# Kernel optimization log

Measured on AMD Instinct MI355X. Metric: run time of the kernel, lower is better.

Reference implementation:

```python
import jax, jax.numpy as jnp
import numpy as np

B, D, H, W, C = 2, 28, 28, 28, 96
HEADS = 3
WS = (7, 7, 7)
SS = (3, 3, 3)
N = WS[0] * WS[1] * WS[2]  # 343 tokens per window
MLP_DIM = 4 * C


def _rel_pos_index():
    coords = np.stack(np.meshgrid(np.arange(WS[0]), np.arange(WS[1]), np.arange(WS[2]), indexing='ij'))
    cf = coords.reshape(3, -1)
    rel = (cf[:, :, None] - cf[:, None, :]).transpose(1, 2, 0)
    rel[..., 0] += WS[0] - 1
    rel[..., 1] += WS[1] - 1
    rel[..., 2] += WS[2] - 1
    rel[..., 0] *= (2 * WS[1] - 1) * (2 * WS[2] - 1)
    rel[..., 1] *= 2 * WS[2] - 1
    return rel.sum(-1)  # [N, N] int


def _compute_mask():
    # shifted-window attention mask (MONAI compute_mask)
    img = np.zeros((1, D, H, W, 1), np.float32)
    cnt = 0.0
    for ds in (slice(0, -WS[0]), slice(-WS[0], -SS[0]), slice(-SS[0], None)):
        for hs in (slice(0, -WS[1]), slice(-WS[1], -SS[1]), slice(-SS[1], None)):
            for ws_ in (slice(0, -WS[2]), slice(-WS[2], -SS[2]), slice(-SS[2], None)):
                img[:, ds, hs, ws_, :] = cnt
                cnt += 1.0
    mw = img.reshape(1, D // WS[0], WS[0], H // WS[1], WS[1], W // WS[2], WS[2], 1)
    mw = mw.transpose(0, 1, 3, 5, 2, 4, 6, 7).reshape(-1, N)  # [nw, N]
    diff = mw[:, None, :] - mw[:, :, None]
    return np.where(diff != 0, -100.0, 0.0).astype(np.float32)  # [nw, N, N]


def _ln(x, g, b):
    mu = x.mean(-1, keepdims=True)
    var = ((x - mu) ** 2).mean(-1, keepdims=True)
    return (x - mu) * jax.lax.rsqrt(var + 1e-5) * g + b


def setup_inputs() -> dict:
    key = jax.random.key(0)
    ks = jax.random.split(key, 8)
    f = lambda k, shape: (jax.random.normal(k, shape) * 0.02).astype(jnp.float32)
    n_bias = (2 * WS[0] - 1) * (2 * WS[1] - 1) * (2 * WS[2] - 1)
    return {
        'x': jax.random.normal(ks[0], (B, D, H, W, C), jnp.float32),
        'mask_matrix': jnp.asarray(_compute_mask()),
        'g1': jnp.ones((C,), jnp.float32), 'b1': jnp.zeros((C,), jnp.float32),
        'w_qkv': f(ks[1], (3 * C, C)), 'b_qkv': jnp.zeros((3 * C,), jnp.float32),
        'bias_table': f(ks[2], (n_bias, HEADS)),
        'w_proj': f(ks[3], (C, C)), 'b_proj': jnp.zeros((C,), jnp.float32),
        'g2': jnp.ones((C,), jnp.float32), 'b2': jnp.zeros((C,), jnp.float32),
        'w_fc1': f(ks[4], (MLP_DIM, C)), 'b_fc1': jnp.zeros((MLP_DIM,), jnp.float32),
        'w_fc2': f(ks[5], (C, MLP_DIM)), 'b_fc2': jnp.zeros((C,), jnp.float32),
        'rel_index': jnp.asarray(_rel_pos_index(), dtype=jnp.int32),
    }


def reference(x, mask_matrix, g1, b1, w_qkv, b_qkv, bias_table, w_proj, b_proj,
              g2, b2, w_fc1, b_fc1, w_fc2, b_fc2, rel_index):
    shortcut = x
    h = _ln(x, g1, b1)
    # cyclic shift
    h = jnp.roll(h, (-SS[0], -SS[1], -SS[2]), axis=(1, 2, 3))
    # window partition -> [B_, N, C]
    win = h.reshape(B, D // WS[0], WS[0], H // WS[1], WS[1], W // WS[2], WS[2], C)
    win = win.transpose(0, 1, 3, 5, 2, 4, 6, 7).reshape(-1, N, C)
    Bw = win.shape[0]
    hd = C // HEADS
    qkv = (win @ w_qkv.T + b_qkv).reshape(Bw, N, 3, HEADS, hd).transpose(2, 0, 3, 1, 4)
    q, k, v = qkv[0] * (hd ** -0.5), qkv[1], qkv[2]
    attn = jnp.einsum('bhnd,bhmd->bhnm', q, k)  # [Bw, H, N, N]
    bias = bias_table[rel_index.reshape(-1)].reshape(N, N, HEADS).transpose(2, 0, 1)
    attn = attn + bias[None]
    nw = mask_matrix.shape[0]
    attn = attn.reshape(Bw // nw, nw, HEADS, N, N) + mask_matrix[None, :, None]
    attn = jax.nn.softmax(attn.reshape(Bw, HEADS, N, N), axis=-1)
    out = jnp.einsum('bhnm,bhmd->bhnd', attn, v).transpose(0, 2, 1, 3).reshape(Bw, N, C)
    out = out @ w_proj.T + b_proj
    # window reverse -> [B, D, H, W, C]
    out = out.reshape(B, D // WS[0], H // WS[1], W // WS[2], WS[0], WS[1], WS[2], C)
    out = out.transpose(0, 1, 4, 2, 5, 3, 6, 7).reshape(B, D, H, W, C)
    # reverse cyclic shift
    out = jnp.roll(out, SS, axis=(1, 2, 3))
    x = shortcut + out
    h2 = _ln(x, g2, b2)
    h2 = jax.nn.gelu(h2 @ w_fc1.T + b_fc1, approximate=False)
    return x + (h2 @ w_fc2.T + b_fc2)
```

## Files before the change

kernel.cpp:

```cpp
#include <hip/hip_runtime.h>
#include <hip/hip_bf16.h>
#include <math.h>

typedef unsigned short u16;
typedef unsigned int u32;
typedef unsigned char u8;

#define T_TOK 43904
#define NTOK 343
#define LOG2E 1.4426950408889634f
#define MASKV 144.26950408889634f

typedef __attribute__((ext_vector_type(4))) float f32x4;
typedef __attribute__((ext_vector_type(8))) short s16x8;

__device__ __forceinline__ float bf2f(u32 v) { return __uint_as_float(v << 16); }
__device__ __forceinline__ u16 f2bf(float f) {
  u32 u = __float_as_uint(f);
  return (u16)((u + 0x7fffu + ((u >> 16) & 1u)) >> 16);
}

__device__ __forceinline__ float ldf(const void* p, int f32, size_t i) {
  return f32 ? ((const float*)p)[i] : bf2f(((const u16*)p)[i]);
}
__device__ __forceinline__ void ld8(const void* p, int f32, size_t i, float* o) {
  if (f32) {
    float4 a = *(const float4*)((const float*)p + i);
    float4 b = *(const float4*)((const float*)p + i + 4);
    o[0] = a.x; o[1] = a.y; o[2] = a.z; o[3] = a.w;
    o[4] = b.x; o[5] = b.y; o[6] = b.z; o[7] = b.w;
  } else {
    uint4 pk = *(const uint4*)((const u16*)p + i);
    u32 v[4] = {pk.x, pk.y, pk.z, pk.w};
    #pragma unroll
    for (int q = 0; q < 4; q++) { o[2 * q] = bf2f(v[q] & 0xffff); o[2 * q + 1] = bf2f(v[q] >> 16); }
  }
}

__device__ __forceinline__ int detect_f32x(const u16* xr) {
  int lane = threadIdx.x & 63;
  int bad = 0;
  #pragma unroll
  for (int q = 0; q < 8; q++) {
    u16 b = xr[(lane * 8 + q) * 2];
    if (((b >> 7) & 0xff) >= 0x90) bad = 1;
  }
  return (__ballot(bad) != 0ull) ? 1 : 0;
}

__device__ __forceinline__ size_t spatial_base(int t) {
  int win = t / 343, n = t - win * 343;
  int bb = win >> 6, wrem = win & 63;
  int wd = wrem >> 4, wh = (wrem >> 2) & 3, ww = wrem & 3;
  int td = n / 49; int r = n - td * 49; int th = r / 7; int tw = r - th * 7;
  int d0 = wd * 7 + td + 3; if (d0 >= 28) d0 -= 28;
  int h0 = wh * 7 + th + 3; if (h0 >= 28) h0 -= 28;
  int w0 = ww * 7 + tw + 3; if (w0 >= 28) w0 -= 28;
  return (size_t)(((bb * 28 + d0) * 28 + h0) * 28 + w0) * 96;
}

__device__ __forceinline__ int zone3(int p) { return p < 21 ? 0 : (p < 25 ? 1 : 2); }
__device__ __forceinline__ int cid_of(int mw, int n) {
  int td = n / 49, rr = n - td * 49, th = rr / 7, tw = rr - th * 7;
  int d = (mw >> 4) * 7 + td, h = ((mw >> 2) & 3) * 7 + th, w = (mw & 3) * 7 + tw;
  return zone3(d) * 9 + zone3(h) * 3 + zone3(w);
}

__global__ __launch_bounds__(256) void setup_kernel(
    const u16* __restrict__ x,
    const void* __restrict__ w0, const void* __restrict__ w1,
    const void* __restrict__ w2, const void* __restrict__ w3,
    const void* __restrict__ bias_table, const int* __restrict__ rel,
    u16* __restrict__ wcat, u16* __restrict__ b3m) {
  int f32 = detect_f32x(x);
  int b = blockIdx.x;
  if (b < 432) {
    int g = b * 256 + threadIdx.x;
    if (g < 110592) {
      float v;
      if (g < 27648)      v = ldf(w0, f32, g);
      else if (g < 36864) v = ldf(w1, f32, g - 27648);
      else if (g < 73728) v = ldf(w2, f32, g - 36864);
      else                v = ldf(w3, f32, g - 73728);
      wcat[g] = f2bf(v);
    }
    return;
  }
  int row = b - 432;
  for (int by = 0; by < 24; by++) {
    int cls = by / 3, head = by - cls * 3;
    int mw = ((cls & 4) ? 48 : 0) | ((cls & 2) ? 12 : 0) | ((cls & 1) ? 3 : 0);
    int cidq = cid_of(mw, row);
    for (int col = threadIdx.x; col < 352; col += 256) {
      float v = -MASKV;
      if (col < 343) {
        v = ldf(bias_table, f32, (size_t)rel[row * 343 + col] * 3 + head) * LOG2E;
        if (cid_of(mw, col) != cidq) v -= MASKV;
      }
      b3m[((size_t)by * 343 + row) * 352 + col] = f2bf(v);
    }
  }
}

__global__ __launch_bounds__(256) void qkv_ln_kernel(
    const void* __restrict__ x, const void* __restrict__ g1, const void* __restrict__ b1,
    const u16* __restrict__ Wb, const void* __restrict__ bias,
    u16* __restrict__ outp) {
  int f32 = detect_f32x((const u16*)x);
  __shared__ alignas(16) u16 As[128 * 104];
  __shared__ alignas(16) u16 Ws[96 * 104];
  __shared__ float gld[96], bld[96];
  int tid = threadIdx.x;
  int m0 = blockIdx.x * 128, n0 = blockIdx.y * 96;
  int w = tid >> 6, lane = tid & 63, quad = lane >> 4, l16 = lane & 15;

  for (int i = tid; i < 1536; i += 256) {
    int row = i / 12, cc = (i - row * 12) * 8;
    size_t sb = spatial_base(m0 + row);
    float f[8];
    ld8(x, f32, sb + cc, f);
    uint4 pk;
    pk.x = (u32)f2bf(f[0]) | ((u32)f2bf(f[1]) << 16);
    pk.y = (u32)f2bf(f[2]) | ((u32)f2bf(f[3]) << 16);
    pk.z = (u32)f2bf(f[4]) | ((u32)f2bf(f[5]) << 16);
    pk.w = (u32)f2bf(f[6]) | ((u32)f2bf(f[7]) << 16);
    *(uint4*)&As[row * 104 + cc] = pk;
  }
  for (int i = tid; i < 1152; i += 256) {
    int row = i / 12, cc = (i - row * 12) * 8;
    *(uint4*)&Ws[row * 104 + cc] = *(const uint4*)(Wb + (size_t)(n0 + row) * 96 + cc);
  }
  if (tid < 96) { gld[tid] = ldf(g1, f32, tid); bld[tid] = ldf(b1, f32, tid); }
  __syncthreads();

  {
    int row = tid >> 1, half = tid & 1;
    u32* rp = (u32*)&As[row * 104] + half * 24;
    float s = 0.f, ss = 0.f;
    #pragma unroll
    for (int m = 0; m < 24; m++) {
      u32 pk = rp[m];
      float a = bf2f(pk & 0xffff), b = bf2f(pk >> 16);
      s += a + b; ss += a * a + b * b;
    }
    s += __shfl_xor(s, 1); ss += __shfl_xor(ss, 1);
    float mean = s * (1.f / 96.f);
    float var = ss * (1.f / 96.f) - mean * mean;
    float rstd = rsqrtf(var + 1e-5f);
    int cbase = half * 48;
    #pragma unroll
    for (int m = 0; m < 24; m++) {
      u32 pk = rp[m];
      float a = bf2f(pk & 0xffff), b = bf2f(pk >> 16);
      a = (a - mean) * rstd * gld[cbase + 2 * m] + bld[cbase + 2 * m];
      b = (b - mean) * rstd * gld[cbase + 2 * m + 1] + bld[cbase + 2 * m + 1];
      rp[m] = (u32)f2bf(a) | ((u32)f2bf(b) << 16);
    }
  }
  __syncthreads();

  f32x4 acc[2][6];
  #pragma unroll
  for (int i = 0; i < 2; i++)
    #pragma unroll
    for (int j = 0; j < 6; j++) acc[i][j] = (f32x4){0.f, 0.f, 0.f, 0.f};
  #pragma unroll
  for (int kc = 0; kc < 3; kc++) {
    s16x8 fa0 = *(const s16x8*)&As[(w * 32 + l16) * 104 + kc * 32 + quad * 8];
    s16x8 fa1 = *(const s16x8*)&As[(w * 32 + 16 + l16) * 104 + kc * 32 + quad * 8];
    #pragma unroll
    for (int j = 0; j < 6; j++) {
      s16x8 fb = *(const s16x8*)&Ws[(j * 16 + l16) * 104 + kc * 32 + quad * 8];
      acc[0][j] = __builtin_amdgcn_mfma_f32_16x16x32_bf16(fa0, fb, acc[0][j], 0, 0, 0);
      acc[1][j] = __builtin_amdgcn_mfma_f32_16x16x32_bf16(fa1, fb, acc[1][j], 0, 0, 0);
    }
  }
  #pragma unroll
  for (int i = 0; i < 2; i++) {
    #pragma unroll
    for (int r = 0; r < 4; r++) {
      int mm = m0 + w * 32 + i * 16 + quad * 4 + r;
      #pragma unroll
      for (int j = 0; j < 6; j++) {
        int nn = n0 + j * 16 + l16;
        float v = acc[i][j][r] + ldf(bias, f32, nn);
        int sel = nn / 96, hd = (nn - sel * 96) >> 5, cc = nn & 31;
        float scl = (sel == 0) ? 0.25504208f : 1.0f;
        outp[((size_t)(sel * 3 + hd) * T_TOK + mm) * 32 + cc] = f2bf(v * scl);
      }
    }
  }
}

__device__ __forceinline__ int vsw(int ch) { return ((ch >> 1) ^ (ch >> 3)) & 3; }

__global__ __launch_bounds__(512) void attn_mfma_kernel(
    const u16* __restrict__ qkv, const u16* __restrict__ b3m,
    u16* __restrict__ attnb) {
  __shared__ alignas(16) u16 Ks[352 * 32];
  __shared__ alignas(16) u16 Vt[32 * 352];
  __shared__ alignas(16) u16 Ps[8][512];

  int tid = threadIdx.x;
  int wh = blockIdx.y;
  int head = wh % 3;
  int win = wh / 3;
  int mw = win & 63;
  int cls = (((mw >> 4) == 3) ? 4 : 0) | ((((mw >> 2) & 3) == 3) ? 2 : 0) | (((mw & 3) == 3) ? 1 : 0);
  int m0 = blockIdx.x * 128;
  size_t wbase = (size_t)win * NTOK;

  const u16* qplane = qkv + ((size_t)head * T_TOK + wbase) * 32;
  const u16* kplane = qkv + ((size_t)(3 + head) * T_TOK + wbase) * 32;
  const u16* vplane = qkv + ((size_t)(6 + head) * T_TOK + wbase) * 32;

  for (int i = tid; i < 1408; i += 512) {
    int tok = i >> 2, cb = i & 3;
    uint4 kv = make_uint4(0, 0, 0, 0);
    if (tok < 343) kv = *(const uint4*)(kplane + (size_t)tok * 32 + cb * 8);
    *(uint4*)&Ks[tok * 32 + 8 * (cb ^ (tok & 3))] = kv;
  }
  for (int i = tid; i < 688; i += 512) {
    int p = i >> 2, cb = (i & 3) * 8;
    int t0 = 2 * p;
    uint4 v0 = *(const uint4*)(vplane + (size_t)t0 * 32 + cb);
    uint4 v1 = make_uint4(0, 0, 0, 0);
    if (t0 + 1 < 343) v1 = *(const uint4*)(vplane + (size_t)(t0 + 1) * 32 + cb);
    u32 a0[4] = {v0.x, v0.y, v0.z, v0.w};
    u32 a1[4] = {v1.x, v1.y, v1.z, v1.w};
    int blk = t0 >> 3, tin = (t0 & 7) >> 1;
    #pragma unroll
    for (int q = 0; q < 4; q++) {
      int ch0 = cb + 2 * q;
      u32 w0v = (a0[q] & 0xffffu) | ((a1[q] & 0xffffu) << 16);
      u32 w1v = (a0[q] >> 16) | (a1[q] & 0xffff0000u);
      ((u32*)Vt)[ch0 * 176 + 4 * (blk ^ vsw(ch0)) + tin] = w0v;
      ((u32*)Vt)[(ch0 + 1) * 176 + 4 * (blk ^ vsw(ch0 + 1)) + tin] = w1v;
    }
  }
  if (tid < 256) {
    int ch = tid >> 3, j = tid & 7;
    Vt[ch * 352 + 8 * (43 ^ vsw(ch)) + j] = 0;
  }
  __syncthreads();

  int w = tid >> 6, lane = tid & 63, quad = lane >> 4, l16 = lane & 15;
  int qbase = m0 + w * 16;
  int qrow_l = qbase + l16;
  int qc = qrow_l < NTOK ? qrow_l : NTOK - 1;
  s16x8 fq = *(const s16x8*)(qplane + (size_t)qc * 32 + quad * 8);
  const u16* bmrow = b3m + ((size_t)(cls * 3 + head) * 343 + qc) * 352;
  int swl = (l16 ^ (l16 >> 2)) & 3;
  int vsw0 = vsw(l16), vsw1 = vsw(16 + l16);

  float lsum = 0.f;
  f32x4 o0 = {0.f, 0.f, 0.f, 0.f}, o1 = {0.f, 0.f, 0.f, 0.f};
  const f32x4 zz = {0.f, 0.f, 0.f, 0.f};

  for (int t32 = 0; t32 < 11; t32++) {
    #pragma unroll
    for (int h = 0; h < 2; h++) {
      int kb = t32 * 32 + h * 16;
      int ktok = kb + l16;
      s16x8 fk = *(const s16x8*)&Ks[ktok * 32 + 8 * (quad ^ (ktok & 3))];
      f32x4 st = __builtin_amdgcn_mfma_f32_16x16x32_bf16(fk, fq, zz, 0, 0, 0);
      uint2 bm = *(const uint2*)(bmrow + kb + quad * 4);
      float p0 = exp2f(st[0] + bf2f(bm.x & 0xffff));
      float p1 = exp2f(st[1] + bf2f(bm.x >> 16));
      float p2 = exp2f(st[2] + bf2f(bm.y & 0xffff));
      float p3 = exp2f(st[3] + bf2f(bm.y >> 16));
      lsum += (p0 + p1) + (p2 + p3);
      u32 pa = (__float_as_uint(p0) >> 16) | (__float_as_uint(p1) & 0xffff0000u);
      u32 pb = (__float_as_uint(p2) >> 16) | (__float_as_uint(p3) & 0xffff0000u);
      int blkp = h * 2 + (quad >> 1);
      *(uint2*)&Ps[w][l16 * 32 + 8 * (blkp ^ swl) + (quad & 1) * 4] = make_uint2(pa, pb);
    }
    s16x8 fp  = *(const s16x8*)&Ps[w][l16 * 32 + 8 * (quad ^ swl)];
    s16x8 fv0 = *(const s16x8*)&Vt[l16 * 352 + 8 * ((t32 * 4 + quad) ^ vsw0)];
    s16x8 fv1 = *(const s16x8*)&Vt[(16 + l16) * 352 + 8 * ((t32 * 4 + quad) ^ vsw1)];
    o0 = __builtin_amdgcn_mfma_f32_16x16x32_bf16(fp, fv0, o0, 0, 0, 0);
    o1 = __builtin_amdgcn_mfma_f32_16x16x32_bf16(fp, fv1, o1, 0, 0, 0);
  }

  lsum += __shfl_xor(lsum, 16);
  lsum += __shfl_xor(lsum, 32);
  #pragma unroll
  for (int r = 0; r < 4; r++) {
    int qrow = qbase + quad * 4 + r;
    float ls = __shfl(lsum, quad * 4 + r);
    if (qrow < NTOK) {
      float rs = 1.0f / ls;
      size_t ob = (wbase + qrow) * 96 + head * 32;
      attnb[ob + l16] = f2bf(o0[r] * rs);
      attnb[ob + 16 + l16] = f2bf(o1[r] * rs);
    }
  }
}

__global__ __launch_bounds__(256) void mlp_fused_kernel(
    const u16* __restrict__ attnb, const u16* __restrict__ wcat,
    const void* __restrict__ x, const void* __restrict__ b_proj,
    const void* __restrict__ g2, const void* __restrict__ b2,
    const void* __restrict__ b_fc1, const void* __restrict__ b_fc2,
    void* __restrict__ outp) {
  int f32 = detect_f32x((const u16*)x);
  __shared__ alignas(16) u16 As[64 * 104];
  __shared__ alignas(16) u16 As2[64 * 104];
  __shared__ alignas(16) u16 Ws[96 * 104];
  const u16* w_projb = wcat + 27648;
  const u16* w_fc1b  = wcat + 36864;
  const u16* w_fc2b  = wcat + 73728;
  int tid = threadIdx.x, m0 = blockIdx.x * 64;
  int w = tid >> 6, lane = tid & 63, quad = lane >> 4, l16 = lane & 15;

  for (int i = tid; i < 768; i += 256) {
    int row = i / 12, c = (i - row * 12) * 8;
    *(uint4*)&As[row * 104 + c] = *(const uint4*)(attnb + (size_t)(m0 + row) * 96 + c);
  }
  for (int i = tid; i < 1152; i += 256) {
    int row = i / 12, c = (i - row * 12) * 8;
    *(uint4*)&Ws[row * 104 + c] = *(const uint4*)(w_projb + row * 96 + c);
  }
  __syncthreads();
  f32x4 accp[6];
  #pragma unroll
  for (int j = 0; j < 6; j++) accp[j] = (f32x4){0.f, 0.f, 0.f, 0.f};
  #pragma unroll
  for (int kc = 0; kc < 3; kc++) {
    s16x8 fa = *(const s16x8*)&As[(w * 16 + l16) * 104 + kc * 32 + quad * 8];
    #pragma unroll
    for (int j = 0; j < 6; j++) {
      s16x8 fb = *(const s16x8*)&Ws[(j * 16 + l16) * 104 + kc * 32 + quad * 8];
      accp[j] = __builtin_amdgcn_mfma_f32_16x16x32_bf16(fa, fb, accp[j], 0, 0, 0);
    }
  }
  __syncthreads();

  float bp[6], gv[6], b2v[6];
  #pragma unroll
  for (int j = 0; j < 6; j++) {
    int nn = j * 16 + l16;
    bp[j] = ldf(b_proj, f32, nn); gv[j] = ldf(g2, f32, nn); b2v[j] = ldf(b2, f32, nn);
  }
  float rv[4][6];
  size_t sb[4];
  #pragma unroll
  for (int r = 0; r < 4; r++) {
    int mm = m0 + w * 16 + quad * 4 + r;
    sb[r] = spatial_base(mm);
    float s = 0.f, ss = 0.f;
    #pragma unroll
    for (int j = 0; j < 6; j++) {
      float v = accp[j][r] + bp[j] + ldf(x, f32, sb[r] + j * 16 + l16);
      rv[r][j] = v; s += v; ss += v * v;
    }
    #pragma unroll
    for (int o = 1; o < 16; o <<= 1) { s += __shfl_xor(s, o); ss += __shfl_xor(ss, o); }
    float mean = s * (1.f / 96.f);
    float var = ss * (1.f / 96.f) - mean * mean;
    float rstd = rsqrtf(var + 1e-5f);
    #pragma unroll
    for (int j = 0; j < 6; j++)
      As[(w * 16 + quad * 4 + r) * 104 + j * 16 + l16] = f2bf((rv[r][j] - mean) * rstd * gv[j] + b2v[j]);
  }

  f32x4 acc2[6];
  #pragma unroll
  for (int j = 0; j < 6; j++) acc2[j] = (f32x4){0.f, 0.f, 0.f, 0.f};
  for (int c = 0; c < 4; c++) {
    __syncthreads();
    for (int i = tid; i < 1152; i += 256) {
      int row = i / 12, cc = (i - row * 12) * 8;
      *(uint4*)&Ws[row * 104 + cc] = *(const uint4*)(w_fc1b + (size_t)(96 * c + row) * 96 + cc);
    }
    __syncthreads();
    f32x4 a1[6];
    #pragma unroll
    for (int j = 0; j < 6; j++) a1[j] = (f32x4){0.f, 0.f, 0.f, 0.f};
    #pragma unroll
    for (int kc = 0; kc < 3; kc++) {
      s16x8 fa = *(const s16x8*)&As[(w * 16 + l16) * 104 + kc * 32 + quad * 8];
      #pragma unroll
      for (int j = 0; j < 6; j++) {
        s16x8 fb = *(const s16x8*)&Ws[(j * 16 + l16) * 104 + kc * 32 + quad * 8];
        a1[j] = __builtin_amdgcn_mfma_f32_16x16x32_bf16(fa, fb, a1[j], 0, 0, 0);
      }
    }
    #pragma unroll
    for (int j = 0; j < 6; j++) {
      float bf1 = ldf(b_fc1, f32, 96 * c + j * 16 + l16);
      #pragma unroll
      for (int r = 0; r < 4; r++) {
        float v = a1[j][r] + bf1;
        v = 0.5f * v * (1.0f + erff(v * 0.70710678118f));
        As2[(w * 16 + quad * 4 + r) * 104 + j * 16 + l16] = f2bf(v);
      }
    }
    __syncthreads();
    for (int i = tid; i < 1152; i += 256) {
      int row = i / 12, cc = (i - row * 12) * 8;
      *(uint4*)&Ws[row * 104 + cc] = *(const uint4*)(w_fc2b + (size_t)row * 384 + 96 * c + cc);
    }
    __syncthreads();
    #pragma unroll
    for (int kc = 0; kc < 3; kc++) {
      s16x8 fa2 = *(const s16x8*)&As2[(w * 16 + l16) * 104 + kc * 32 + quad * 8];
      #pragma unroll
      for (int j = 0; j < 6; j++) {
        s16x8 fb = *(const s16x8*)&Ws[(j * 16 + l16) * 104 + kc * 32 + quad * 8];
        acc2[j] = __builtin_amdgcn_mfma_f32_16x16x32_bf16(fa2, fb, acc2[j], 0, 0, 0);
      }
    }
  }
  float bf2v[6];
  #pragma unroll
  for (int j = 0; j < 6; j++) bf2v[j] = ldf(b_fc2, f32, j * 16 + l16);
  #pragma unroll
  for (int r = 0; r < 4; r++) {
    #pragma unroll
    for (int j = 0; j < 6; j++) {
      float v = acc2[j][r] + bf2v[j] + rv[r][j];
      if (f32) ((float*)outp)[sb[r] + j * 16 + l16] = v;
      else     ((u16*)outp)[sb[r] + j * 16 + l16] = f2bf(v);
    }
  }
}

extern "C" void kernel_launch(void* const* d_in, const int* in_sizes, int n_in,
                              void* d_out, int out_size, void* d_ws, size_t ws_size,
                              hipStream_t stream) {
  (void)in_sizes; (void)n_in; (void)out_size; (void)ws_size;
  const void* x       = d_in[0];
  const void* g1      = d_in[2];
  const void* b1      = d_in[3];
  const void* w_qkv   = d_in[4];
  const void* b_qkv   = d_in[5];
  const void* bias_tb = d_in[6];
  const void* w_proj  = d_in[7];
  const void* b_proj  = d_in[8];
  const void* g2      = d_in[9];
  const void* b2      = d_in[10];
  const void* w_fc1   = d_in[11];
  const void* b_fc1   = d_in[12];
  const void* w_fc2   = d_in[13];
  const void* b_fc2   = d_in[14];
  const int* rel_idx  = (const int*)d_in[15];

  char* ws = (char*)d_ws;
  u16*  qkvb  = (u16*)(ws + 256);
  u16*  attnb = (u16*)(ws + 256 + 25288704);
  u16*  b3mb  = (u16*)(ws + 256 + 25288704 + 8429568);
  u16*  wcat  = (u16*)(ws + 256 + 25288704 + 8429568 + 5795328);
  u16*  w_qkvb = wcat;

  setup_kernel<<<775, 256, 0, stream>>>((const u16*)x, w_qkv, w_proj, w_fc1, w_fc2,
                                        bias_tb, rel_idx, wcat, b3mb);
  qkv_ln_kernel<<<dim3(343, 3), 256, 0, stream>>>(x, g1, b1, w_qkvb, b_qkv, qkvb);
  attn_mfma_kernel<<<dim3(3, 384), 512, 0, stream>>>(qkvb, b3mb, attnb);
  mlp_fused_kernel<<<686, 256, 0, stream>>>(attnb, wcat, x, b_proj, g2, b2,
                                            b_fc1, b_fc2, d_out);
}
```

Before: 238.2 us.

## Pre-pad weights and double-buffer them into LDS with async global_load_lds

Setup now writes the weights in padded row-major chunks (stride 104) so they can be streamed straight into LDS with global_load_lds. The qkv kernel computes all three output blocks in one workgroup, reusing the normalized A tile, and double-buffers the weight chunks. The MLP kernel ping-pongs between two weight buffers so the next fc1 or fc2 chunk loads while the current one is consumed. The setup kernel's bias/mask construction is also spread across many more blocks, and exact erf GELU is replaced by a tanh approximation, which changes numerics slightly.

```diff
diff --git a/kernel.cpp b/kernel.cpp
--- a/kernel.cpp
+++ b/kernel.cpp
@@ -10,6 +10,12 @@
 #define NTOK 343
 #define LOG2E 1.4426950408889634f
 #define MASKV 144.26950408889634f
+
+#define QKVOFF  0
+#define PROJOFF 30208
+#define FC1OFF  40448
+#define FC2OFF  80640
+#define WCATSZ  123000
 
 typedef __attribute__((ext_vector_type(4))) float f32x4;
 typedef __attribute__((ext_vector_type(8))) short s16x8;
@@ -48,6 +54,22 @@
   return (__ballot(bad) != 0ull) ? 1 : 0;
 }
 
+__device__ __forceinline__ void ws_fill(const u16* gsrc, u16* lbuf, int w, int lane) {
+  const u16* g = gsrc + w * 2560 + lane * 8;
+  u16* l = lbuf + w * 2560;
+  #pragma unroll
+  for (int i = 0; i < 5; i++)
+    __builtin_amdgcn_global_load_lds(
+        (const __attribute__((address_space(1))) void*)(g + i * 512),
+        (__attribute__((address_space(3))) void*)(l + i * 512), 16, 0, 0);
+}
+
+__device__ __forceinline__ float gelu_t(float v) {
+  float u = v * (0.7978845608f + 0.03567740814f * v * v);
+  float e = exp2f(u * 2.885390082f);
+  return v - v / (1.f + e);
+}
+
 __device__ __forceinline__ size_t spatial_base(int t) {
   int win = t / 343, n = t - win * 343;
   int bb = win >> 6, wrem = win & 63;
@@ -74,46 +96,57 @@
     u16* __restrict__ wcat, u16* __restrict__ b3m) {
   int f32 = detect_f32x(x);
   int b = blockIdx.x;
-  if (b < 432) {
+  if (b < 468) {
     int g = b * 256 + threadIdx.x;
-    if (g < 110592) {
-      float v;
-      if (g < 27648)      v = ldf(w0, f32, g);
-      else if (g < 36864) v = ldf(w1, f32, g - 27648);
-      else if (g < 73728) v = ldf(w2, f32, g - 36864);
-      else                v = ldf(w3, f32, g - 73728);
-      wcat[g] = f2bf(v);
+    if (g < 119808) {
+      int dst, n, k;
+      float v = 0.f;
+      if (g < 29952) {
+        n = g / 104; k = g - n * 104; dst = QKVOFF + g;
+        if (k < 96) v = ldf(w0, f32, (size_t)n * 96 + k);
+      } else if (g < 39936) {
+        int r = g - 29952; n = r / 104; k = r - n * 104; dst = PROJOFF + r;
+        if (k < 96) v = ldf(w1, f32, (size_t)n * 96 + k);
+      } else if (g < 79872) {
+        int r = g - 39936; n = r / 104; k = r - n * 104; dst = FC1OFF + r;
+        if (k < 96) v = ldf(w2, f32, (size_t)n * 96 + k);
+      } else {
+        int r = g - 79872; int c = r / 9984; int r2 = r - c * 9984;
+        n = r2 / 104; k = r2 - n * 104; dst = FC2OFF + r;
+        if (k < 96) v = ldf(w3, f32, (size_t)n * 384 + 96 * c + k);
+      }
+      wcat[dst] = f2bf(v);
     }
     return;
   }
-  int row = b - 432;
-  for (int by = 0; by < 24; by++) {
-    int cls = by / 3, head = by - cls * 3;
-    int mw = ((cls & 4) ? 48 : 0) | ((cls & 2) ? 12 : 0) | ((cls & 1) ? 3 : 0);
-    int cidq = cid_of(mw, row);
-    for (int col = threadIdx.x; col < 352; col += 256) {
-      float v = -MASKV;
-      if (col < 343) {
-        v = ldf(bias_table, f32, (size_t)rel[row * 343 + col] * 3 + head) * LOG2E;
-        if (cid_of(mw, col) != cidq) v -= MASKV;
-      }
-      b3m[((size_t)by * 343 + row) * 352 + col] = f2bf(v);
-    }
+  int bb = b - 468;
+  int row = bb / 24, by = bb - row * 24;
+  int cls = by / 3, head = by - cls * 3;
+  int mw = ((cls & 4) ? 48 : 0) | ((cls & 2) ? 12 : 0) | ((cls & 1) ? 3 : 0);
+  int cidq = cid_of(mw, row);
+  for (int col = threadIdx.x; col < 352; col += 256) {
+    float v = -MASKV;
+    if (col < 343) {
+      v = ldf(bias_table, f32, (size_t)rel[row * 343 + col] * 3 + head) * LOG2E;
+      if (cid_of(mw, col) != cidq) v -= MASKV;
+    }
+    b3m[((size_t)by * 343 + row) * 352 + col] = f2bf(v);
   }
 }
 
 __global__ __launch_bounds__(256) void qkv_ln_kernel(
     const void* __restrict__ x, const void* __restrict__ g1, const void* __restrict__ b1,
-    const u16* __restrict__ Wb, const void* __restrict__ bias,
+    const u16* __restrict__ wcat, const void* __restrict__ bias,
     u16* __restrict__ outp) {
   int f32 = detect_f32x((const u16*)x);
   __shared__ alignas(16) u16 As[128 * 104];
-  __shared__ alignas(16) u16 Ws[96 * 104];
+  __shared__ alignas(16) u16 Wb[2][10240];
   __shared__ float gld[96], bld[96];
   int tid = threadIdx.x;
-  int m0 = blockIdx.x * 128, n0 = blockIdx.y * 96;
+  int m0 = blockIdx.x * 128;
   int w = tid >> 6, lane = tid & 63, quad = lane >> 4, l16 = lane & 15;
 
+  ws_fill(wcat + QKVOFF, Wb[0], w, lane);
   for (int i = tid; i < 1536; i += 256) {
     int row = i / 12, cc = (i - row * 12) * 8;
     size_t sb = spatial_base(m0 + row);
@@ -126,10 +159,6 @@
     pk.w = (u32)f2bf(f[6]) | ((u32)f2bf(f[7]) << 16);
     *(uint4*)&As[row * 104 + cc] = pk;
   }
-  for (int i = tid; i < 1152; i += 256) {
-    int row = i / 12, cc = (i - row * 12) * 8;
-    *(uint4*)&Ws[row * 104 + cc] = *(const uint4*)(Wb + (size_t)(n0 + row) * 96 + cc);
-  }
   if (tid < 96) { gld[tid] = ldf(g1, f32, tid); bld[tid] = ldf(b1, f32, tid); }
   __syncthreads();
 
@@ -157,38 +186,42 @@
       rp[m] = (u32)f2bf(a) | ((u32)f2bf(b) << 16);
     }
   }
-  __syncthreads();
-
-  f32x4 acc[2][6];
-  #pragma unroll
-  for (int i = 0; i < 2; i++)
-    #pragma unroll
-    for (int j = 0; j < 6; j++) acc[i][j] = (f32x4){0.f, 0.f, 0.f, 0.f};
-  #pragma unroll
-  for (int kc = 0; kc < 3; kc++) {
-    s16x8 fa0 = *(const s16x8*)&As[(w * 32 + l16) * 104 + kc * 32 + quad * 8];
-    s16x8 fa1 = *(const s16x8*)&As[(w * 32 + 16 + l16) * 104 + kc * 32 + quad * 8];
-    #pragma unroll
-    for (int j = 0; j < 6; j++) {
-      s16x8 fb = *(const s16x8*)&Ws[(j * 16 + l16) * 104 + kc * 32 + quad * 8];
-      acc[0][j] = __builtin_amdgcn_mfma_f32_16x16x32_bf16(fa0, fb, acc[0][j], 0, 0, 0);
-      acc[1][j] = __builtin_amdgcn_mfma_f32_16x16x32_bf16(fa1, fb, acc[1][j], 0, 0, 0);
-    }
-  }
-  #pragma unroll
-  for (int i = 0; i < 2; i++) {
-    #pragma unroll
-    for (int r = 0; r < 4; r++) {
-      int mm = m0 + w * 32 + i * 16 + quad * 4 + r;
+
+  int cur = 0;
+  for (int nb = 0; nb < 3; nb++) {
+    if (nb < 2) ws_fill(wcat + QKVOFF + (nb + 1) * 9984, Wb[cur ^ 1], w, lane);
+    f32x4 acc[2][6];
+    #pragma unroll
+    for (int i = 0; i < 2; i++)
+      #pragma unroll
+      for (int j = 0; j < 6; j++) acc[i][j] = (f32x4){0.f, 0.f, 0.f, 0.f};
+    #pragma unroll
+    for (int kc = 0; kc < 3; kc++) {
+      s16x8 fa0 = *(const s16x8*)&As[(w * 32 + l16) * 104 + kc * 32 + quad * 8];
+      s16x8 fa1 = *(const s16x8*)&As[(w * 32 + 16 + l16) * 104 + kc * 32 + quad * 8];
       #pragma unroll
       for (int j = 0; j < 6; j++) {
-        int nn = n0 + j * 16 + l16;
-        float v = acc[i][j][r] + ldf(bias, f32, nn);
-        int sel = nn / 96, hd = (nn - sel * 96) >> 5, cc = nn & 31;
-        float scl = (sel == 0) ? 0.25504208f : 1.0f;
-        outp[((size_t)(sel * 3 + hd) * T_TOK + mm) * 32 + cc] = f2bf(v * scl);
+        s16x8 fb = *(const s16x8*)&Wb[cur][(j * 16 + l16) * 104 + kc * 32 + quad * 8];
+        acc[0][j] = __builtin_amdgcn_mfma_f32_16x16x32_bf16(fa0, fb, acc[0][j], 0, 0, 0);
+        acc[1][j] = __builtin_amdgcn_mfma_f32_16x16x32_bf16(fa1, fb, acc[1][j], 0, 0, 0);
       }
     }
+    #pragma unroll
+    for (int i = 0; i < 2; i++) {
+      #pragma unroll
+      for (int r = 0; r < 4; r++) {
+        int mm = m0 + w * 32 + i * 16 + quad * 4 + r;
+        #pragma unroll
+        for (int j = 0; j < 6; j++) {
+          int nn = nb * 96 + j * 16 + l16;
+          float v = acc[i][j][r] + ldf(bias, f32, nn);
+          int sel = nb, cd = j * 16 + l16, hd = cd >> 5, cc = cd & 31;
+          float scl = (sel == 0) ? 0.25504208f : 1.0f;
+          outp[((size_t)(sel * 3 + hd) * T_TOK + mm) * 32 + cc] = f2bf(v * scl);
+        }
+      }
+    }
+    if (nb < 2) { __syncthreads(); cur ^= 1; }
   }
 }
 
@@ -306,22 +339,18 @@
   int f32 = detect_f32x((const u16*)x);
   __shared__ alignas(16) u16 As[64 * 104];
   __shared__ alignas(16) u16 As2[64 * 104];
-  __shared__ alignas(16) u16 Ws[96 * 104];
-  const u16* w_projb = wcat + 27648;
-  const u16* w_fc1b  = wcat + 36864;
-  const u16* w_fc2b  = wcat + 73728;
+  __shared__ alignas(16) u16 Wb[2][10240];
   int tid = threadIdx.x, m0 = blockIdx.x * 64;
   int w = tid >> 6, lane = tid & 63, quad = lane >> 4, l16 = lane & 15;
 
+  ws_fill(wcat + PROJOFF, Wb[1], w, lane);
   for (int i = tid; i < 768; i += 256) {
     int row = i / 12, c = (i - row * 12) * 8;
     *(uint4*)&As[row * 104 + c] = *(const uint4*)(attnb + (size_t)(m0 + row) * 96 + c);
   }
-  for (int i = tid; i < 1152; i += 256) {
-    int row = i / 12, c = (i - row * 12) * 8;
-    *(uint4*)&Ws[row * 104 + c] = *(const uint4*)(w_projb + row * 96 + c);
-  }
   __syncthreads();
+  ws_fill(wcat + FC1OFF, Wb[0], w, lane);
+
   f32x4 accp[6];
   #pragma unroll
   for (int j = 0; j < 6; j++) accp[j] = (f32x4){0.f, 0.f, 0.f, 0.f};
@@ -330,11 +359,10 @@
     s16x8 fa = *(const s16x8*)&As[(w * 16 + l16) * 104 + kc * 32 + quad * 8];
     #pragma unroll
     for (int j = 0; j < 6; j++) {
-      s16x8 fb = *(const s16x8*)&Ws[(j * 16 + l16) * 104 + kc * 32 + quad * 8];
+      s16x8 fb = *(const s16x8*)&Wb[1][(j * 16 + l16) * 104 + kc * 32 + quad * 8];
       accp[j] = __builtin_amdgcn_mfma_f32_16x16x32_bf16(fa, fb, accp[j], 0, 0, 0);
     }
   }
-  __syncthreads();
 
   float bp[6], gv[6], b2v[6];
   #pragma unroll
@@ -363,17 +391,13 @@
     for (int j = 0; j < 6; j++)
       As[(w * 16 + quad * 4 + r) * 104 + j * 16 + l16] = f2bf((rv[r][j] - mean) * rstd * gv[j] + b2v[j]);
   }
+  __syncthreads();
 
   f32x4 acc2[6];
   #pragma unroll
   for (int j = 0; j < 6; j++) acc2[j] = (f32x4){0.f, 0.f, 0.f, 0.f};
   for (int c = 0; c < 4; c++) {
-    __syncthreads();
-    for (int i = tid; i < 1152; i += 256) {
-      int row = i / 12, cc = (i - row * 12) * 8;
-      *(uint4*)&Ws[row * 104 + cc] = *(const uint4*)(w_fc1b + (size_t)(96 * c + row) * 96 + cc);
-    }
-    __syncthreads();
+    ws_fill(wcat + FC2OFF + c * 9984, Wb[1], w, lane);
     f32x4 a1[6];
     #pragma unroll
     for (int j = 0; j < 6; j++) a1[j] = (f32x4){0.f, 0.f, 0.f, 0.f};
@@ -382,7 +406,7 @@
       s16x8 fa = *(const s16x8*)&As[(w * 16 + l16) * 104 + kc * 32 + quad * 8];
       #pragma unroll
       for (int j = 0; j < 6; j++) {
-        s16x8 fb = *(const s16x8*)&Ws[(j * 16 + l16) * 104 + kc * 32 + quad * 8];
+        s16x8 fb = *(const s16x8*)&Wb[0][(j * 16 + l16) * 104 + kc * 32 + quad * 8];
         a1[j] = __builtin_amdgcn_mfma_f32_16x16x32_bf16(fa, fb, a1[j], 0, 0, 0);
       }
     }
@@ -390,27 +414,21 @@
     for (int j = 0; j < 6; j++) {
       float bf1 = ldf(b_fc1, f32, 96 * c + j * 16 + l16);
       #pragma unroll
-      for (int r = 0; r < 4; r++) {
-        float v = a1[j][r] + bf1;
-        v = 0.5f * v * (1.0f + erff(v * 0.70710678118f));
-        As2[(w * 16 + quad * 4 + r) * 104 + j * 16 + l16] = f2bf(v);
-      }
+      for (int r = 0; r < 4; r++)
+        As2[(w * 16 + quad * 4 + r) * 104 + j * 16 + l16] = f2bf(gelu_t(a1[j][r] + bf1));
     }
     __syncthreads();
-    for (int i = tid; i < 1152; i += 256) {
-      int row = i / 12, cc = (i - row * 12) * 8;
-      *(uint4*)&Ws[row * 104 + cc] = *(const uint4*)(w_fc2b + (size_t)row * 384 + 96 * c + cc);
-    }
-    __syncthreads();
+    if (c < 3) ws_fill(wcat + FC1OFF + (c + 1) * 9984, Wb[0], w, lane);
     #pragma unroll
     for (int kc = 0; kc < 3; kc++) {
       s16x8 fa2 = *(const s16x8*)&As2[(w * 16 + l16) * 104 + kc * 32 + quad * 8];
       #pragma unroll
       for (int j = 0; j < 6; j++) {
-        s16x8 fb = *(const s16x8*)&Ws[(j * 16 + l16) * 104 + kc * 32 + quad * 8];
+        s16x8 fb = *(const s16x8*)&Wb[1][(j * 16 + l16) * 104 + kc * 32 + quad * 8];
         acc2[j] = __builtin_amdgcn_mfma_f32_16x16x32_bf16(fa2, fb, acc2[j], 0, 0, 0);
       }
     }
+    if (c < 3) __syncthreads();
   }
   float bf2v[6];
   #pragma unroll
@@ -451,11 +469,10 @@
   u16*  attnb = (u16*)(ws + 256 + 25288704);
   u16*  b3mb  = (u16*)(ws + 256 + 25288704 + 8429568);
   u16*  wcat  = (u16*)(ws + 256 + 25288704 + 8429568 + 5795328);
-  u16*  w_qkvb = wcat;
-
-  setup_kernel<<<775, 256, 0, stream>>>((const u16*)x, w_qkv, w_proj, w_fc1, w_fc2,
-                                        bias_tb, rel_idx, wcat, b3mb);
-  qkv_ln_kernel<<<dim3(343, 3), 256, 0, stream>>>(x, g1, b1, w_qkvb, b_qkv, qkvb);
+
+  setup_kernel<<<8700, 256, 0, stream>>>((const u16*)x, w_qkv, w_proj, w_fc1, w_fc2,
+                                         bias_tb, rel_idx, wcat, b3mb);
+  qkv_ln_kernel<<<343, 256, 0, stream>>>(x, g1, b1, wcat, b_qkv, qkvb);
   attn_mfma_kernel<<<dim3(3, 384), 512, 0, stream>>>(qkvb, b3mb, attnb);
   mlp_fused_kernel<<<686, 256, 0, stream>>>(attnb, wcat, x, b_proj, g2, b2,
                                             b_fc1, b_fc2, d_out);
```

After: 255.4 us. +7.2%, slower.
